# Kernel tuning notes

Measured on AMD Instinct MI355X. Metric: run time of the kernel, lower is better.

## Reference

```python
import jax, jax.numpy as jnp
import numpy as np

B, S, H, L = 256, 512, 1024, 30


def setup_inputs() -> dict:
    key = jax.random.key(0)
    ks = jax.random.split(key, 10)
    x = jax.random.normal(ks[0], (B, S, H), jnp.float32)
    # strictly increasing indices -> non-empty spans [i0,i1) and [i2,i3)
    entity_idx = jnp.sort(jax.random.randint(ks[1], (B, 4), 0, S - 4), axis=1) + jnp.arange(4)
    sc = 0.02
    return {
        "x": x,
        "entity_idx": entity_idx,
        "W_cls": jax.random.normal(ks[2], (H, H), jnp.float32) * sc,
        "b_cls": jnp.zeros((H,), jnp.float32),
        "W_e1": jax.random.normal(ks[3], (H, H), jnp.float32) * sc,
        "b_e1": jnp.zeros((H,), jnp.float32),
        "W_e2": jax.random.normal(ks[4], (H, H), jnp.float32) * sc,
        "b_e2": jnp.zeros((H,), jnp.float32),
        "W_d1": jax.random.normal(ks[5], (3 * H, H), jnp.float32) * sc,
        "b_d1": jnp.zeros((H,), jnp.float32),
        "W_d2": jax.random.normal(ks[6], (H, H), jnp.float32) * sc,
        "b_d2": jnp.zeros((H,), jnp.float32),
        "W_out": jax.random.normal(ks[7], (H, L), jnp.float32) * sc,
        "b_out": jnp.zeros((L,), jnp.float32),
    }


def _span_mean(x, lo, hi):
    # x: [B,S,H]; lo,hi: [B] -> mean over tokens in [lo,hi) per sample
    pos = jnp.arange(x.shape[1])
    m = ((pos[None, :] >= lo[:, None]) & (pos[None, :] < hi[:, None])).astype(x.dtype)  # [B,S]
    s = jnp.einsum("bs,bsh->bh", m, x)
    cnt = jnp.maximum(m.sum(axis=-1, keepdims=True), 1.0)
    return s / cnt


def reference(x, entity_idx, W_cls, b_cls, W_e1, b_e1, W_e2, b_e2,
              W_d1, b_d1, W_d2, b_d2, W_out, b_out):
    sub = _span_mean(x, entity_idx[:, 0], entity_idx[:, 1])  # [B,H]
    obj = _span_mean(x, entity_idx[:, 2], entity_idx[:, 3])  # [B,H]
    x0 = jnp.tanh(x[:, 0, :]) @ W_cls + b_cls
    e1 = jnp.tanh(sub) @ W_e1 + b_e1
    e2 = jnp.tanh(obj) @ W_e2 + b_e2
    h = jnp.concatenate([x0, e1, e2], axis=1)  # [B,3H]
    h = h @ W_d1 + b_d1  # dropout is identity in eval mode
    h = h @ W_d2 + b_d2
    return h @ W_out + b_out  # [B,L]
```

## Files before the change

### kernel.cpp

```cpp
#include <hip/hip_runtime.h>
#include <hip/hip_bf16.h>


#define B_ 256
#define S_ 512
#define H_ 1024
#define L_ 30
#define NCHUNK 8
#define KSPLIT 8

__global__ __launch_bounds__(256) void span_partial_kernel(
    const float* __restrict__ x, const int* __restrict__ eidx,
    float* __restrict__ Pspan) {
  const int b = blockIdx.x;
  const int chunk = blockIdx.y;
  const int role = blockIdx.z;
  const int lo = eidx[b * 4 + 2 * role];
  const int hi = eidx[b * 4 + 2 * role + 1];
  int s0 = max(lo, chunk * 64);
  int s1 = min(hi, chunk * 64 + 64);
  if (s0 >= s1) return;

  const int col = threadIdx.x * 4;
  const float* base = x + (size_t)b * S_ * H_ + col;
  float ax0 = 0.f, ay0 = 0.f, az0 = 0.f, aw0 = 0.f;
  float ax1 = 0.f, ay1 = 0.f, az1 = 0.f, aw1 = 0.f;
  int s = s0;
  for (; s + 2 <= s1; s += 2) {
    float4 v0 = *(const float4*)(base + (size_t)s * H_);
    float4 v1 = *(const float4*)(base + (size_t)(s + 1) * H_);
    ax0 += v0.x; ay0 += v0.y; az0 += v0.z; aw0 += v0.w;
    ax1 += v1.x; ay1 += v1.y; az1 += v1.z; aw1 += v1.w;
  }
  if (s < s1) {
    float4 v0 = *(const float4*)(base + (size_t)s * H_);
    ax0 += v0.x; ay0 += v0.y; az0 += v0.z; aw0 += v0.w;
  }
  float4 o;
  o.x = ax0 + ax1; o.y = ay0 + ay1; o.z = az0 + az1; o.w = aw0 + aw1;
  *(float4*)(Pspan + (((size_t)b * 2 + role) * NCHUNK + chunk) * H_ + col) = o;
}

__device__ __forceinline__ void foldgemm_body(
    const float* __restrict__ A, const float* __restrict__ Smat,
    float* __restrict__ Cp, int M, int rowblk, int ks, int out_row_off) {
  __shared__ float As[64][132];
  const int t = threadIdx.x;
  const int k0 = ks * 128;

#pragma unroll
  for (int i = 0; i < 32; ++i) {
    int idx = t + i * 64;
    int r = idx >> 5;
    int c = (idx & 31) << 2;
    float4 v = *(const float4*)(A + (size_t)(rowblk + r) * H_ + k0 + c);
    *(float4*)&As[r][c] = v;
  }
  __syncthreads();

  float acc[30];
#pragma unroll
  for (int n = 0; n < 30; ++n) acc[n] = 0.f;

  for (int kk = 0; kk < 128; kk += 4) {
    float4 a = *(const float4*)&As[t][kk];
    const float* Sr = Smat + (size_t)(k0 + kk) * 30;
#pragma unroll
    for (int n = 0; n < 30; ++n) {
      acc[n] += a.x * Sr[n] + a.y * Sr[n + 30] + a.z * Sr[n + 60] + a.w * Sr[n + 90];
    }
  }

  float* Crow = Cp + ((size_t)ks * M + out_row_off + rowblk + t) * 30;
#pragma unroll
  for (int n = 0; n < 30; ++n) Crow[n] = acc[n];
}

__global__ __launch_bounds__(64) void foldgemm_single(
    const float* __restrict__ A, const float* __restrict__ Smat,
    float* __restrict__ Cp, int M) {
  foldgemm_body(A, Smat, Cp, M, blockIdx.x * 64, blockIdx.y, 0);
}

__global__ __launch_bounds__(64) void foldgemm_tri(
    const float* __restrict__ A0, const float* __restrict__ A1,
    const float* __restrict__ A2, const float* __restrict__ Wd1o,
    float* __restrict__ Cp) {
  const int z = blockIdx.z;
  const float* A = (z == 0) ? A0 : ((z == 1) ? A1 : A2);
  const float* Smat = Wd1o + (size_t)z * H_ * 30;
  foldgemm_body(A, Smat, Cp, 3 * H_, blockIdx.x * 64, blockIdx.y, z * H_);
}

__global__ __launch_bounds__(256) void reduce8_kernel(
    const float* __restrict__ Cp, float* __restrict__ C, int N) {
  int i = blockIdx.x * 256 + threadIdx.x;
  if (i >= N) return;
  float s = 0.f;
#pragma unroll
  for (int ks = 0; ks < KSPLIT; ++ks) s += Cp[(size_t)ks * N + i];
  C[i] = s;
}

__global__ __launch_bounds__(256) void bias_kernel(
    const float* __restrict__ b_out, const float* __restrict__ b_d2,
    const float* __restrict__ W_out, const float* __restrict__ b_d1,
    const float* __restrict__ P1, const float* __restrict__ b_cls,
    const float* __restrict__ b_e1, const float* __restrict__ b_e2,
    const float* __restrict__ Wd1o, float* __restrict__ btot) {
  const int n = blockIdx.x;
  const int t = threadIdx.x;
  __shared__ float red[256];
  float s = 0.f;
  for (int k = t; k < H_; k += 256) {
    s += b_d2[k] * W_out[(size_t)k * L_ + n];
    s += b_d1[k] * P1[(size_t)k * L_ + n];
    s += b_cls[k] * Wd1o[(size_t)k * L_ + n];
    s += b_e1[k] * Wd1o[(size_t)(H_ + k) * L_ + n];
    s += b_e2[k] * Wd1o[(size_t)(2 * H_ + k) * L_ + n];
  }
  red[t] = s;
  __syncthreads();
  for (int off = 128; off > 0; off >>= 1) {
    if (t < off) red[t] += red[t + off];
    __syncthreads();
  }
  if (t == 0) btot[n] = red[0] + b_out[n];
}

__global__ __launch_bounds__(256) void final_kernel(
    const float* __restrict__ x, const int* __restrict__ eidx,
    const float* __restrict__ Pspan, const float* __restrict__ Wf,
    const float* __restrict__ btot, float* __restrict__ out) {
  __shared__ float Ts[3 * H_];
  __shared__ float red[8][30];
  const int b = blockIdx.x;
  const int t = threadIdx.x;
  const int col = t * 4;

  {
    float4 v = *(const float4*)(x + (size_t)b * S_ * H_ + col);
    Ts[col + 0] = tanhf(v.x);
    Ts[col + 1] = tanhf(v.y);
    Ts[col + 2] = tanhf(v.z);
    Ts[col + 3] = tanhf(v.w);
  }
#pragma unroll
  for (int role = 0; role < 2; ++role) {
    const int lo = eidx[b * 4 + 2 * role];
    const int hi = eidx[b * 4 + 2 * role + 1];
    const int c0 = lo >> 6;
    const int c1 = (hi - 1) >> 6;
    float ax = 0.f, ay = 0.f, az = 0.f, aw = 0.f;
    for (int c = c0; c <= c1; ++c) {
      float4 v = *(const float4*)(Pspan + (((size_t)b * 2 + role) * NCHUNK + c) * H_ + col);
      ax += v.x; ay += v.y; az += v.z; aw += v.w;
    }
    const float inv = 1.0f / (float)(hi - lo);
    float* Td = Ts + (1 + role) * H_ + col;
    Td[0] = tanhf(ax * inv);
    Td[1] = tanhf(ay * inv);
    Td[2] = tanhf(az * inv);
    Td[3] = tanhf(aw * inv);
  }
  __syncthreads();

  if (t < 240) {
    const int n = t % 30, p = t / 30;
    const int k0 = p * 384;
    float s = 0.f;
#pragma unroll 4
    for (int k = k0; k < k0 + 384; ++k) s += Ts[k] * Wf[(size_t)k * L_ + n];
    red[p][n] = s;
  }
  __syncthreads();
  if (t < L_) {
    float s = btot[t];
#pragma unroll
    for (int p = 0; p < 8; ++p) s += red[p][t];
    out[(size_t)b * L_ + t] = s;
  }
}

extern "C" void kernel_launch(void* const* d_in, const int* in_sizes, int n_in,
                              void* d_out, int out_size, void* d_ws, size_t ws_size,
                              hipStream_t stream) {
  const float* x = (const float*)d_in[0];
  const int* eidx = (const int*)d_in[1];
  const float* W_cls = (const float*)d_in[2];
  const float* b_cls = (const float*)d_in[3];
  const float* W_e1 = (const float*)d_in[4];
  const float* b_e1 = (const float*)d_in[5];
  const float* W_e2 = (const float*)d_in[6];
  const float* b_e2 = (const float*)d_in[7];
  const float* W_d1 = (const float*)d_in[8];
  const float* b_d1 = (const float*)d_in[9];
  const float* W_d2 = (const float*)d_in[10];
  const float* b_d2 = (const float*)d_in[11];
  const float* W_out = (const float*)d_in[12];
  const float* b_out = (const float*)d_in[13];
  float* out = (float*)d_out;

  float* ws = (float*)d_ws;
  float* Pspan = ws;
  float* P1p   = Pspan + 4194304;
  float* P1    = P1p + 245760;
  float* Wp    = P1 + 30720;
  float* Wd1o  = Wp + 737280;
  float* Wp2   = Wd1o + 92160;
  float* Wfold = Wp2 + 737280;
  float* btot  = Wfold + 92160;

  span_partial_kernel<<<dim3(B_, NCHUNK, 2), 256, 0, stream>>>(x, eidx, Pspan);

  foldgemm_single<<<dim3(H_ / 64, KSPLIT), 64, 0, stream>>>(W_d2, W_out, P1p, H_);
  reduce8_kernel<<<(H_ * 30 + 255) / 256, 256, 0, stream>>>(P1p, P1, H_ * 30);

  foldgemm_single<<<dim3(3 * H_ / 64, KSPLIT), 64, 0, stream>>>(W_d1, P1, Wp, 3 * H_);
  reduce8_kernel<<<(3 * H_ * 30 + 255) / 256, 256, 0, stream>>>(Wp, Wd1o, 3 * H_ * 30);

  foldgemm_tri<<<dim3(H_ / 64, KSPLIT, 3), 64, 0, stream>>>(W_cls, W_e1, W_e2, Wd1o, Wp2);
  reduce8_kernel<<<(3 * H_ * 30 + 255) / 256, 256, 0, stream>>>(Wp2, Wfold, 3 * H_ * 30);

  bias_kernel<<<L_, 256, 0, stream>>>(b_out, b_d2, W_out, b_d1, P1,
                                      b_cls, b_e1, b_e2, Wd1o, btot);

  final_kernel<<<B_, 256, 0, stream>>>(x, eidx, Pspan, Wfold, btot, out);
}
```

Before: 167.6 us.

## Restructure weight-folding GEMMs with 32-way K split, LDS-staged S, fused bias reduce

Replaces the fold GEMM with a kernel that splits K into 32 chunks of 32, stages the small S matrix transposed in shared memory, and has each thread compute two rows. This raises the block count and moves S reads from global to LDS. The reduction kernel now sums 32 partials, and the bias kernel is folded into the last reduce launch to save one launch. In exchange the partial-sum buffers are four times larger and the reduce passes read more data.

```diff
diff --git a/kernel.cpp b/kernel.cpp
--- a/kernel.cpp
+++ b/kernel.cpp
@@ -7,7 +7,8 @@
 #define H_ 1024
 #define L_ 30
 #define NCHUNK 8
-#define KSPLIT 8
+#define KC 32
+#define KS 32
 
 __global__ __launch_bounds__(256) void span_partial_kernel(
     const float* __restrict__ x, const int* __restrict__ eidx,
@@ -41,75 +42,80 @@
   *(float4*)(Pspan + (((size_t)b * 2 + role) * NCHUNK + chunk) * H_ + col) = o;
 }
 
-__device__ __forceinline__ void foldgemm_body(
-    const float* __restrict__ A, const float* __restrict__ Smat,
-    float* __restrict__ Cp, int M, int rowblk, int ks, int out_row_off) {
-  __shared__ float As[64][132];
+__global__ __launch_bounds__(64) void fold32_kernel(
+    const float* __restrict__ A0, const float* __restrict__ A1,
+    const float* __restrict__ A2, const float* __restrict__ Smat,
+    long s_z_stride, float* __restrict__ Cp, int Mtot, int zshift) {
+  __shared__ float As[128][36];
+  __shared__ float St[30][36];
   const int t = threadIdx.x;
-  const int k0 = ks * 128;
-
-#pragma unroll
-  for (int i = 0; i < 32; ++i) {
+  const int bx = blockIdx.x;
+  const int ks = blockIdx.y;
+  const int k0 = ks * KC;
+  const int z = bx >> zshift;
+  const int arowbase = (bx - (z << zshift)) * 128;
+  const int crowbase = bx * 128;
+  const float* A = (z == 0) ? A0 : ((z == 1) ? A1 : A2);
+  const float* S = Smat + (size_t)z * s_z_stride;
+
+#pragma unroll
+  for (int i = 0; i < 16; ++i) {
     int idx = t + i * 64;
-    int r = idx >> 5;
-    int c = (idx & 31) << 2;
-    float4 v = *(const float4*)(A + (size_t)(rowblk + r) * H_ + k0 + c);
-    *(float4*)&As[r][c] = v;
-  }
-  __syncthreads();
-
-  float acc[30];
-#pragma unroll
-  for (int n = 0; n < 30; ++n) acc[n] = 0.f;
-
-  for (int kk = 0; kk < 128; kk += 4) {
-    float4 a = *(const float4*)&As[t][kk];
-    const float* Sr = Smat + (size_t)(k0 + kk) * 30;
+    int r = idx >> 3;
+    int c4 = (idx & 7) << 2;
+    float4 v = *(const float4*)(A + (size_t)(arowbase + r) * H_ + k0 + c4);
+    *(float4*)&As[r][c4] = v;
+  }
+#pragma unroll
+  for (int i = 0; i < 15; ++i) {
+    int idx = t + i * 64;
+    int k = idx / 30, n = idx - k * 30;
+    St[n][k] = S[(size_t)(k0 + k) * L_ + n];
+  }
+  __syncthreads();
+
+  float acc0[30], acc1[30];
+#pragma unroll
+  for (int n = 0; n < 30; ++n) { acc0[n] = 0.f; acc1[n] = 0.f; }
+
+#pragma unroll
+  for (int kk = 0; kk < KC; kk += 4) {
+    float4 a0 = *(const float4*)&As[t][kk];
+    float4 a1 = *(const float4*)&As[t + 64][kk];
 #pragma unroll
     for (int n = 0; n < 30; ++n) {
-      acc[n] += a.x * Sr[n] + a.y * Sr[n + 30] + a.z * Sr[n + 60] + a.w * Sr[n + 90];
+      float4 s4 = *(const float4*)&St[n][kk];
+      acc0[n] += a0.x * s4.x + a0.y * s4.y + a0.z * s4.z + a0.w * s4.w;
+      acc1[n] += a1.x * s4.x + a1.y * s4.y + a1.z * s4.z + a1.w * s4.w;
     }
   }
 
-  float* Crow = Cp + ((size_t)ks * M + out_row_off + rowblk + t) * 30;
-#pragma unroll
-  for (int n = 0; n < 30; ++n) Crow[n] = acc[n];
-}
-
-__global__ __launch_bounds__(64) void foldgemm_single(
-    const float* __restrict__ A, const float* __restrict__ Smat,
-    float* __restrict__ Cp, int M) {
-  foldgemm_body(A, Smat, Cp, M, blockIdx.x * 64, blockIdx.y, 0);
-}
-
-__global__ __launch_bounds__(64) void foldgemm_tri(
-    const float* __restrict__ A0, const float* __restrict__ A1,
-    const float* __restrict__ A2, const float* __restrict__ Wd1o,
-    float* __restrict__ Cp) {
-  const int z = blockIdx.z;
-  const float* A = (z == 0) ? A0 : ((z == 1) ? A1 : A2);
-  const float* Smat = Wd1o + (size_t)z * H_ * 30;
-  foldgemm_body(A, Smat, Cp, 3 * H_, blockIdx.x * 64, blockIdx.y, z * H_);
-}
-
-__global__ __launch_bounds__(256) void reduce8_kernel(
-    const float* __restrict__ Cp, float* __restrict__ C, int N) {
-  int i = blockIdx.x * 256 + threadIdx.x;
-  if (i >= N) return;
-  float s = 0.f;
-#pragma unroll
-  for (int ks = 0; ks < KSPLIT; ++ks) s += Cp[(size_t)ks * N + i];
-  C[i] = s;
-}
-
-__global__ __launch_bounds__(256) void bias_kernel(
+  float* c0 = Cp + ((size_t)ks * Mtot + crowbase + t) * L_;
+  float* c1 = Cp + ((size_t)ks * Mtot + crowbase + t + 64) * L_;
+#pragma unroll
+  for (int n = 0; n < 30; ++n) { c0[n] = acc0[n]; c1[n] = acc1[n]; }
+}
+
+__global__ __launch_bounds__(256) void reduce32_kernel(
+    const float* __restrict__ src, float* __restrict__ dst, int N, int nred,
+    int do_bias,
     const float* __restrict__ b_out, const float* __restrict__ b_d2,
     const float* __restrict__ W_out, const float* __restrict__ b_d1,
     const float* __restrict__ P1, const float* __restrict__ b_cls,
     const float* __restrict__ b_e1, const float* __restrict__ b_e2,
     const float* __restrict__ Wd1o, float* __restrict__ btot) {
-  const int n = blockIdx.x;
   const int t = threadIdx.x;
+  if ((int)blockIdx.x < nred) {
+    int i = blockIdx.x * 256 + t;
+    if (i >= N) return;
+    float s = 0.f;
+#pragma unroll 8
+    for (int p = 0; p < KS; ++p) s += src[(size_t)p * N + i];
+    dst[i] = s;
+    return;
+  }
+  if (!do_bias) return;
+  const int n = blockIdx.x - nred;
   __shared__ float red[256];
   float s = 0.f;
   for (int k = t; k < H_; k += 256) {
@@ -204,26 +210,31 @@
   float* ws = (float*)d_ws;
   float* Pspan = ws;
   float* P1p   = Pspan + 4194304;
-  float* P1    = P1p + 245760;
+  float* P1    = P1p + 983040;
   float* Wp    = P1 + 30720;
-  float* Wd1o  = Wp + 737280;
+  float* Wd1o  = Wp + 2949120;
   float* Wp2   = Wd1o + 92160;
-  float* Wfold = Wp2 + 737280;
+  float* Wfold = Wp2 + 2949120;
   float* btot  = Wfold + 92160;
 
   span_partial_kernel<<<dim3(B_, NCHUNK, 2), 256, 0, stream>>>(x, eidx, Pspan);
 
-  foldgemm_single<<<dim3(H_ / 64, KSPLIT), 64, 0, stream>>>(W_d2, W_out, P1p, H_);
-  reduce8_kernel<<<(H_ * 30 + 255) / 256, 256, 0, stream>>>(P1p, P1, H_ * 30);
-
-  foldgemm_single<<<dim3(3 * H_ / 64, KSPLIT), 64, 0, stream>>>(W_d1, P1, Wp, 3 * H_);
-  reduce8_kernel<<<(3 * H_ * 30 + 255) / 256, 256, 0, stream>>>(Wp, Wd1o, 3 * H_ * 30);
-
-  foldgemm_tri<<<dim3(H_ / 64, KSPLIT, 3), 64, 0, stream>>>(W_cls, W_e1, W_e2, Wd1o, Wp2);
-  reduce8_kernel<<<(3 * H_ * 30 + 255) / 256, 256, 0, stream>>>(Wp2, Wfold, 3 * H_ * 30);
-
-  bias_kernel<<<L_, 256, 0, stream>>>(b_out, b_d2, W_out, b_d1, P1,
-                                      b_cls, b_e1, b_e2, Wd1o, btot);
+  fold32_kernel<<<dim3(H_ / 128, KS), 64, 0, stream>>>(
+      W_d2, W_d2, W_d2, W_out, 0, P1p, H_, 30);
+  reduce32_kernel<<<120, 256, 0, stream>>>(P1p, P1, H_ * L_, 120, 0,
+      nullptr, nullptr, nullptr, nullptr, nullptr, nullptr, nullptr, nullptr,
+      nullptr, nullptr);
+
+  fold32_kernel<<<dim3(3 * H_ / 128, KS), 64, 0, stream>>>(
+      W_d1, W_d1, W_d1, P1, 0, Wp, 3 * H_, 30);
+  reduce32_kernel<<<360, 256, 0, stream>>>(Wp, Wd1o, 3 * H_ * L_, 360, 0,
+      nullptr, nullptr, nullptr, nullptr, nullptr, nullptr, nullptr, nullptr,
+      nullptr, nullptr);
+
+  fold32_kernel<<<dim3(3 * H_ / 128, KS), 64, 0, stream>>>(
+      W_cls, W_e1, W_e2, Wd1o, (long)H_ * L_, Wp2, 3 * H_, 3);
+  reduce32_kernel<<<390, 256, 0, stream>>>(Wp2, Wfold, 3 * H_ * L_, 360, 1,
+      b_out, b_d2, W_out, b_d1, P1, b_cls, b_e1, b_e2, Wd1o, btot);
 
   final_kernel<<<B_, 256, 0, stream>>>(x, eidx, Pspan, Wfold, btot, out);
 }
```

Result: slower. 337.3 us (+101.2%).

## Replace split-K fold GEMMs with per-output dot kernels and fuse bias fold

Applied to the files above, without the earlier changes.

Swaps the split-K shared-memory fold GEMMs and their reduction kernels for simple kernels where each thread computes one output element as a full K=1024 dot product. The bias-folding kernel is merged into the last fold kernel, and its three partial sums are added in the final kernel. This cuts the launch count from 9 to 5 and drops the partial-sum workspace traffic. In exchange, each thread runs a long serial loop with row-strided reads of A that coalesce poorly, and a 1024-step serial reduction per output.

```diff
diff --git a/kernel.cpp b/kernel.cpp
--- a/kernel.cpp
+++ b/kernel.cpp
@@ -7,7 +7,6 @@
 #define H_ 1024
 #define L_ 30
 #define NCHUNK 8
-#define KSPLIT 8
 
 __global__ __launch_bounds__(256) void span_partial_kernel(
     const float* __restrict__ x, const int* __restrict__ eidx,
@@ -41,97 +40,64 @@
   *(float4*)(Pspan + (((size_t)b * 2 + role) * NCHUNK + chunk) * H_ + col) = o;
 }
 
-__device__ __forceinline__ void foldgemm_body(
-    const float* __restrict__ A, const float* __restrict__ Smat,
-    float* __restrict__ Cp, int M, int rowblk, int ks, int out_row_off) {
-  __shared__ float As[64][132];
-  const int t = threadIdx.x;
-  const int k0 = ks * 128;
-
-#pragma unroll
-  for (int i = 0; i < 32; ++i) {
-    int idx = t + i * 64;
-    int r = idx >> 5;
-    int c = (idx & 31) << 2;
-    float4 v = *(const float4*)(A + (size_t)(rowblk + r) * H_ + k0 + c);
-    *(float4*)&As[r][c] = v;
-  }
-  __syncthreads();
-
-  float acc[30];
-#pragma unroll
-  for (int n = 0; n < 30; ++n) acc[n] = 0.f;
-
-  for (int kk = 0; kk < 128; kk += 4) {
-    float4 a = *(const float4*)&As[t][kk];
-    const float* Sr = Smat + (size_t)(k0 + kk) * 30;
-#pragma unroll
-    for (int n = 0; n < 30; ++n) {
-      acc[n] += a.x * Sr[n] + a.y * Sr[n + 30] + a.z * Sr[n + 60] + a.w * Sr[n + 90];
-    }
-  }
-
-  float* Crow = Cp + ((size_t)ks * M + out_row_off + rowblk + t) * 30;
-#pragma unroll
-  for (int n = 0; n < 30; ++n) Crow[n] = acc[n];
+__global__ __launch_bounds__(256) void fold_rows_kernel(
+    const float* __restrict__ A, const float* __restrict__ S,
+    float* __restrict__ C, int Mtot) {
+  int idx = blockIdx.x * 256 + threadIdx.x;
+  if (idx >= Mtot * L_) return;
+  int m = idx / L_, n = idx - m * L_;
+  const float* a = A + (size_t)m * H_;
+  const float* s = S + n;
+  float acc = 0.f;
+#pragma unroll 8
+  for (int k = 0; k < H_; ++k) acc += a[k] * s[(size_t)k * L_];
+  C[idx] = acc;
 }
 
-__global__ __launch_bounds__(64) void foldgemm_single(
-    const float* __restrict__ A, const float* __restrict__ Smat,
-    float* __restrict__ Cp, int M) {
-  foldgemm_body(A, Smat, Cp, M, blockIdx.x * 64, blockIdx.y, 0);
-}
-
-__global__ __launch_bounds__(64) void foldgemm_tri(
-    const float* __restrict__ A0, const float* __restrict__ A1,
-    const float* __restrict__ A2, const float* __restrict__ Wd1o,
-    float* __restrict__ Cp) {
-  const int z = blockIdx.z;
-  const float* A = (z == 0) ? A0 : ((z == 1) ? A1 : A2);
-  const float* Smat = Wd1o + (size_t)z * H_ * 30;
-  foldgemm_body(A, Smat, Cp, 3 * H_, blockIdx.x * 64, blockIdx.y, z * H_);
-}
-
-__global__ __launch_bounds__(256) void reduce8_kernel(
-    const float* __restrict__ Cp, float* __restrict__ C, int N) {
-  int i = blockIdx.x * 256 + threadIdx.x;
-  if (i >= N) return;
-  float s = 0.f;
-#pragma unroll
-  for (int ks = 0; ks < KSPLIT; ++ks) s += Cp[(size_t)ks * N + i];
-  C[i] = s;
-}
-
-__global__ __launch_bounds__(256) void bias_kernel(
-    const float* __restrict__ b_out, const float* __restrict__ b_d2,
-    const float* __restrict__ W_out, const float* __restrict__ b_d1,
-    const float* __restrict__ P1, const float* __restrict__ b_cls,
-    const float* __restrict__ b_e1, const float* __restrict__ b_e2,
-    const float* __restrict__ Wd1o, float* __restrict__ btot) {
-  const int n = blockIdx.x;
-  const int t = threadIdx.x;
-  __shared__ float red[256];
-  float s = 0.f;
-  for (int k = t; k < H_; k += 256) {
-    s += b_d2[k] * W_out[(size_t)k * L_ + n];
-    s += b_d1[k] * P1[(size_t)k * L_ + n];
-    s += b_cls[k] * Wd1o[(size_t)k * L_ + n];
-    s += b_e1[k] * Wd1o[(size_t)(H_ + k) * L_ + n];
-    s += b_e2[k] * Wd1o[(size_t)(2 * H_ + k) * L_ + n];
+__global__ __launch_bounds__(256) void foldC_kernel(
+    const float* __restrict__ Wcls, const float* __restrict__ We1,
+    const float* __restrict__ We2, const float* __restrict__ Wd1o,
+    const float* __restrict__ Wout, const float* __restrict__ P1,
+    const float* __restrict__ b_cls, const float* __restrict__ b_e1,
+    const float* __restrict__ b_e2, const float* __restrict__ b_d1,
+    const float* __restrict__ b_d2,
+    float* __restrict__ Wfold, float* __restrict__ rbias) {
+  int idx = blockIdx.x * 256 + threadIdx.x;
+  if (idx < 3 * H_ * L_) {
+    int m = idx / L_, n = idx - m * L_;
+    int z = m >> 10, r = m & (H_ - 1);
+    const float* A = (z == 0) ? Wcls : (z == 1) ? We1 : We2;
+    const float* a = A + (size_t)r * H_;
+    const float* s = Wd1o + (size_t)z * H_ * L_ + n;
+    float acc = 0.f;
+#pragma unroll 8
+    for (int k = 0; k < H_; ++k) acc += a[k] * s[(size_t)k * L_];
+    Wfold[idx] = acc;
+    return;
   }
-  red[t] = s;
-  __syncthreads();
-  for (int off = 128; off > 0; off >>= 1) {
-    if (t < off) red[t] += red[t + off];
-    __syncthreads();
+  int extra = idx - 3 * H_ * L_;
+  if (extra >= 3 * L_) return;
+  int r = extra / L_, n = extra - r * L_;
+  float acc = 0.f;
+  if (r == 0) {
+    for (int k = 0; k < H_; ++k) {
+      acc += b_cls[k] * Wd1o[(size_t)k * L_ + n]
+           + b_e1[k] * Wd1o[(size_t)(H_ + k) * L_ + n]
+           + b_e2[k] * Wd1o[(size_t)(2 * H_ + k) * L_ + n];
+    }
+  } else if (r == 1) {
+    for (int k = 0; k < H_; ++k) acc += b_d1[k] * P1[(size_t)k * L_ + n];
+  } else {
+    for (int k = 0; k < H_; ++k) acc += b_d2[k] * Wout[(size_t)k * L_ + n];
   }
-  if (t == 0) btot[n] = red[0] + b_out[n];
+  rbias[extra] = acc;
 }
 
 __global__ __launch_bounds__(256) void final_kernel(
     const float* __restrict__ x, const int* __restrict__ eidx,
     const float* __restrict__ Pspan, const float* __restrict__ Wf,
-    const float* __restrict__ btot, float* __restrict__ out) {
+    const float* __restrict__ b_out, const float* __restrict__ rbias,
+    float* __restrict__ out) {
   __shared__ float Ts[3 * H_];
   __shared__ float red[8][30];
   const int b = blockIdx.x;
@@ -175,7 +141,7 @@
   }
   __syncthreads();
   if (t < L_) {
-    float s = btot[t];
+    float s = b_out[t] + rbias[t] + rbias[L_ + t] + rbias[2 * L_ + t];
 #pragma unroll
     for (int p = 0; p < 8; ++p) s += red[p][t];
     out[(size_t)b * L_ + t] = s;
@@ -203,27 +169,20 @@
 
   float* ws = (float*)d_ws;
   float* Pspan = ws;
-  float* P1p   = Pspan + 4194304;
-  float* P1    = P1p + 245760;
-  float* Wp    = P1 + 30720;
-  float* Wd1o  = Wp + 737280;
-  float* Wp2   = Wd1o + 92160;
-  float* Wfold = Wp2 + 737280;
-  float* btot  = Wfold + 92160;
+  float* P1    = Pspan + 4194304;
+  float* Wd1o  = P1 + 30720;
+  float* Wfold = Wd1o + 92160;
+  float* rbias = Wfold + 92160;
 
   span_partial_kernel<<<dim3(B_, NCHUNK, 2), 256, 0, stream>>>(x, eidx, Pspan);
 
-  foldgemm_single<<<dim3(H_ / 64, KSPLIT), 64, 0, stream>>>(W_d2, W_out, P1p, H_);
-  reduce8_kernel<<<(H_ * 30 + 255) / 256, 256, 0, stream>>>(P1p, P1, H_ * 30);
+  fold_rows_kernel<<<(H_ * L_ + 255) / 256, 256, 0, stream>>>(W_d2, W_out, P1, H_);
 
-  foldgemm_single<<<dim3(3 * H_ / 64, KSPLIT), 64, 0, stream>>>(W_d1, P1, Wp, 3 * H_);
-  reduce8_kernel<<<(3 * H_ * 30 + 255) / 256, 256, 0, stream>>>(Wp, Wd1o, 3 * H_ * 30);
+  fold_rows_kernel<<<(3 * H_ * L_ + 255) / 256, 256, 0, stream>>>(W_d1, P1, Wd1o, 3 * H_);
 
-  foldgemm_tri<<<dim3(H_ / 64, KSPLIT, 3), 64, 0, stream>>>(W_cls, W_e1, W_e2, Wd1o, Wp2);
-  reduce8_kernel<<<(3 * H_ * 30 + 255) / 256, 256, 0, stream>>>(Wp2, Wfold, 3 * H_ * 30);
+  foldC_kernel<<<(3 * H_ * L_ + 3 * L_ + 255) / 256, 256, 0, stream>>>(
+      W_cls, W_e1, W_e2, Wd1o, W_out, P1,
+      b_cls, b_e1, b_e2, b_d1, b_d2, Wfold, rbias);
 
-  bias_kernel<<<L_, 256, 0, stream>>>(b_out, b_d2, W_out, b_d1, P1,
-                                      b_cls, b_e1, b_e2, Wd1o, btot);
-
-  final_kernel<<<B_, 256, 0, stream>>>(x, eidx, Pspan, Wfold, btot, out);
+  final_kernel<<<B_, 256, 0, stream>>>(x, eidx, Pspan, Wfold, b_out, rbias, out);
 }
```

New measurement: 333.5 us. 99.0% more time.
